# Performance work log

Measured on AMD Instinct MI355X. Metric: run time of the kernel, lower is better.

## Reference

```python
import jax, jax.numpy as jnp
import numpy as np

HEAD_SIZE = 128
N_Q_HEADS = 32
N_KV_HEADS = 8
ROPE_THETA = 1000000.0
RMS_EPS = 1e-6


def rms_norm(x, w, eps=RMS_EPS):
    # normalize over last dim in fp32, like Qwen3RMSNorm
    xf = x.astype(jnp.float32)
    var = jnp.mean(xf * xf, axis=-1, keepdims=True)
    return w * (xf * jax.lax.rsqrt(var + eps)).astype(x.dtype)


def rope_cache(T, dim, theta=ROPE_THETA):
    half = dim // 2
    inv_freq = 1.0 / theta ** (jnp.arange(half, dtype=jnp.float32) / half)
    freqs = jnp.arange(T, dtype=jnp.float32)[:, None] * inv_freq[None, :]  # [T, half]
    emb = jnp.concatenate([freqs, freqs], axis=-1)  # [T, dim]
    return jnp.cos(emb), jnp.sin(emb)


def rotate_half(x):
    x1, x2 = jnp.split(x, 2, axis=-1)
    return jnp.concatenate([-x2, x1], axis=-1)


def setup_inputs() -> dict:
    key = jax.random.key(0)
    ks = jax.random.split(key, 5)
    B, T, C = 2, 2048, 4096
    s = 0.02
    return {
        "hidden_states": jax.random.normal(ks[0], (B, T, C), jnp.float32),
        "wq": jax.random.normal(ks[1], (N_Q_HEADS * HEAD_SIZE, C), jnp.float32) * s,
        "wk": jax.random.normal(ks[2], (N_KV_HEADS * HEAD_SIZE, C), jnp.float32) * s,
        "wv": jax.random.normal(ks[3], (N_KV_HEADS * HEAD_SIZE, C), jnp.float32) * s,
        "wo": jax.random.normal(ks[4], (C, N_Q_HEADS * HEAD_SIZE), jnp.float32) * s,
        "q_norm_w": jnp.ones((HEAD_SIZE,), jnp.float32),
        "k_norm_w": jnp.ones((HEAD_SIZE,), jnp.float32),
    }


def reference(hidden_states, wq, wk, wv, wo, q_norm_w, k_norm_w):
    B, T, C = hidden_states.shape
    D = HEAD_SIZE
    groups = N_Q_HEADS // N_KV_HEADS
    scale = D ** -0.5

    # projections -> [B, H, T, D]
    q = (hidden_states @ wq.T).reshape(B, T, N_Q_HEADS, D)
    k = (hidden_states @ wk.T).reshape(B, T, N_KV_HEADS, D)
    v = (hidden_states @ wv.T).reshape(B, T, N_KV_HEADS, D)

    q = rms_norm(q, q_norm_w).transpose(0, 2, 1, 3)
    k = rms_norm(k, k_norm_w).transpose(0, 2, 1, 3)
    v = v.transpose(0, 2, 1, 3)

    cos, sin = rope_cache(T, D)  # [T, D]
    cos = cos[None, None]  # broadcast over batch, heads
    sin = sin[None, None]
    q = q * cos + rotate_half(q) * sin
    k = k * cos + rotate_half(k) * sin

    # GQA repeat_kv: [B, Hkv, T, D] -> [B, Hq, T, D]
    k = jnp.repeat(k, groups, axis=1)
    v = jnp.repeat(v, groups, axis=1)

    # causal SDPA
    scores = jnp.einsum("bhqd,bhkd->bhqk", q, k) * scale
    causal = jnp.tril(jnp.ones((T, T), bool))
    scores = jnp.where(causal[None, None], scores, -jnp.inf)
    probs = jax.nn.softmax(scores, axis=-1)
    attn = jnp.einsum("bhqk,bhkd->bhqd", probs, v)

    attn = attn.transpose(0, 2, 1, 3).reshape(B, T, N_Q_HEADS * D)
    return attn @ wo.T
```

## Files before the change

kernel.cpp:

```cpp
#include <hip/hip_runtime.h>
#include <math.h>

typedef unsigned short u16;
typedef __attribute__((ext_vector_type(8))) short short8;
typedef __attribute__((ext_vector_type(4))) float f32x4;
typedef __attribute__((ext_vector_type(16))) float f32x16;

#define AS1 __attribute__((address_space(1)))
#define AS3 __attribute__((address_space(3)))

__device__ __forceinline__ void gload_lds16(const u16* g, u16* l) {
  __builtin_amdgcn_global_load_lds((AS1 void*)g, (AS3 void*)l, 16, 0, 0);
}

__device__ __forceinline__ float bf2f(u16 u) {
  union { unsigned i; float f; } c; c.i = ((unsigned)u) << 16; return c.f;
}
__device__ __forceinline__ u16 f2bf(float f) {
  union { float f; unsigned i; } c; c.f = f;
  unsigned r = c.i + 0x7fffu + ((c.i >> 16) & 1u);
  return (u16)(r >> 16);
}

__global__ __launch_bounds__(256)
void cvt_f32_bf16_k(const float* __restrict__ src, u16* __restrict__ dst, int n8)
{
  int i = blockIdx.x * blockDim.x + threadIdx.x;
  const int stride = gridDim.x * blockDim.x;
  for (; i < n8; i += stride) {
    float4 a = ((const float4*)src)[2 * i];
    float4 b = ((const float4*)src)[2 * i + 1];
    short8 o;
    o[0] = (short)f2bf(a.x); o[1] = (short)f2bf(a.y);
    o[2] = (short)f2bf(a.z); o[3] = (short)f2bf(a.w);
    o[4] = (short)f2bf(b.x); o[5] = (short)f2bf(b.y);
    o[6] = (short)f2bf(b.z); o[7] = (short)f2bf(b.w);
    ((short8*)dst)[i] = o;
  }
}

__global__ __launch_bounds__(256)
void cvt_batch4(const float* __restrict__ s0, u16* __restrict__ d0,
                const float* __restrict__ s1, u16* __restrict__ d1,
                const float* __restrict__ s2, u16* __restrict__ d2,
                const float* __restrict__ s3, u16* __restrict__ d3)
{
  int i = blockIdx.x * blockDim.x + threadIdx.x;
  const int stride = gridDim.x * blockDim.x;
  for (; i < 5242880; i += stride) {
    const float* s; u16* d; int j;
    if (i < 2097152)      { s = s0; d = d0; j = i; }
    else if (i < 4194304) { s = s1; d = d1; j = i - 2097152; }
    else if (i < 4718592) { s = s2; d = d2; j = i - 4194304; }
    else                  { s = s3; d = d3; j = i - 4718592; }
    float4 a = ((const float4*)s)[2 * j];
    float4 b = ((const float4*)s)[2 * j + 1];
    short8 o;
    o[0] = (short)f2bf(a.x); o[1] = (short)f2bf(a.y);
    o[2] = (short)f2bf(a.z); o[3] = (short)f2bf(a.w);
    o[4] = (short)f2bf(b.x); o[5] = (short)f2bf(b.y);
    o[6] = (short)f2bf(b.z); o[7] = (short)f2bf(b.w);
    ((short8*)d)[j] = o;
  }
}

#define MFMA16(a, b, c) __builtin_amdgcn_mfma_f32_16x16x32_bf16((a), (b), (c), 0, 0, 0)

#define STAGE_H(panel, h, t, ldsb)                                          \
  { const u16* s_ = (panel) + (size_t)((h) * 128) * 4096 + (t) * 64;        \
    gload_lds16(s_,                   (ldsb) + ldst0);                      \
    gload_lds16(s_ + (size_t)64*4096, (ldsb) + 4096 + ldst0); }

#define PHASE(MB, STAGE_STMT, TAIL)                                         \
  {                                                                         \
    short8 a0k0 = *(const short8*)(aB + (MB)*1024 + aoff0);                 \
    short8 a0k1 = *(const short8*)(aB + (MB)*1024 + (aoff0 ^ 32));          \
    short8 a1k0 = *(const short8*)(aB + ((MB)+1)*1024 + aoff0);             \
    short8 a1k1 = *(const short8*)(aB + ((MB)+1)*1024 + (aoff0 ^ 32));      \
    STAGE_STMT                                                              \
    __builtin_amdgcn_s_barrier();                                           \
    asm volatile("s_waitcnt lgkmcnt(0)" ::: "memory");                      \
    __builtin_amdgcn_s_setprio(1);                                          \
    _Pragma("unroll")                                                       \
    for (int n = 0; n < 4; ++n) {                                           \
      acc[(MB)][n]   = MFMA16(a0k0, br[n][0], acc[(MB)][n]);                \
      acc[(MB)][n]   = MFMA16(a0k1, br[n][1], acc[(MB)][n]);                \
      acc[(MB)+1][n] = MFMA16(a1k0, br[n][0], acc[(MB)+1][n]);              \
      acc[(MB)+1][n] = MFMA16(a1k1, br[n][1], acc[(MB)+1][n]);              \
    }                                                                       \
    __builtin_amdgcn_s_setprio(0);                                          \
    TAIL                                                                    \
    __builtin_amdgcn_s_barrier();                                           \
  }

#define KTILE(BUF, T)                                                       \
  {                                                                         \
    const u16* aB = sA + (BUF) * 16384 + wr * 8192;                         \
    const u16* bB = sB + (BUF) * 16384 + (wc >> 1) * 8192;                  \
    u16* aO = sA + ((BUF) ^ 1) * 16384;                                     \
    u16* bO = sB + (BUF) * 16384;                                           \
    const bool st1 = (T) + 1 < NT, st2 = (T) + 2 < NT;                      \
    short8 br[4][2];                                                        \
    _Pragma("unroll")                                                       \
    for (int n = 0; n < 4; ++n) {                                           \
      br[n][0] = *(const short8*)(bB + n * 1024 + boff0);                   \
      br[n][1] = *(const short8*)(bB + n * 1024 + (boff0 ^ 32));            \
    }                                                                       \
    PHASE(0, if (st1) STAGE_H(aS, 0, (T) + 1, aO);, ;)                      \
    PHASE(2, if (st1) STAGE_H(aS, 1, (T) + 1, aO + 8192);, ;)               \
    PHASE(4, if (st2) STAGE_H(bS, 0, (T) + 2, bO);, ;)                      \
    PHASE(6, if (st2) STAGE_H(bS, 1, (T) + 2, bO + 8192);,                  \
          if ((T) < NT - 2) { asm volatile("s_waitcnt vmcnt(4)" ::: "memory"); } \
          else              { asm volatile("s_waitcnt vmcnt(0)" ::: "memory"); }) \
  }

template<int MODE, typename OutT>
__global__ __launch_bounds__(512, 2)
void gemm256(const u16* __restrict__ A, const u16* __restrict__ W0,
             const u16* __restrict__ W1, const u16* __restrict__ W2,
             OutT* __restrict__ C)
{
  constexpr int K = 4096;
  constexpr int NT = K / 64;
  constexpr int LDC = (MODE == 0) ? 6144 : 4096;
  constexpr int NBM = 16;
  constexpr int NBN = (MODE == 0) ? 24 : 16;
  constexpr int NWG = NBM * NBN;

  __shared__ __align__(16) u16 sA[2 * 16384];
  __shared__ __align__(16) u16 sB[2 * 16384];

  const int tid = threadIdx.x;
  const int wid = tid >> 6, lane = tid & 63;
  const int g = lane >> 4, li = lane & 15;
  const int wr = wid >> 2, wc = wid & 3;

  const int bid = blockIdx.x;
  const int wg = (bid & 7) * (NWG / 8) + (bid >> 3);
  const int bm = wg % NBM, bn = wg / NBM;
  const int n0 = bn * 256;

  const u16* Wp; int nrow0;
  if (MODE == 0) {
    if (n0 < 4096)      { Wp = W0; nrow0 = n0; }
    else if (n0 < 5120) { Wp = W1; nrow0 = n0 - 4096; }
    else                { Wp = W2; nrow0 = n0 - 5120; }
  } else { Wp = W0; nrow0 = n0; }

  const int r0 = tid >> 3;
  const int sc0 = (tid & 7) ^ (r0 & 7);
  const u16* aS = A  + (size_t)(bm * 256 + r0) * K + sc0 * 8;
  const u16* bS = Wp + (size_t)(nrow0   + r0) * K + sc0 * 8;
  const int ldst0 = wid * 512;

  const int aoff0 = li * 64 + ((g ^ (li & 7)) * 8);
  const int boff0 = (wc & 1) * 4096 + aoff0;

  f32x4 acc[8][4] = {};

  STAGE_H(bS, 0, 0, sB);
  STAGE_H(bS, 1, 0, sB + 8192);
  STAGE_H(aS, 0, 0, sA);
  STAGE_H(aS, 1, 0, sA + 8192);
  STAGE_H(bS, 0, 1, sB + 16384);
  STAGE_H(bS, 1, 1, sB + 24576);
  asm volatile("s_waitcnt vmcnt(4)" ::: "memory");
  __builtin_amdgcn_s_barrier();

  for (int t = 0; t < NT; t += 2) {
    KTILE(0, t)
    KTILE(1, t + 1)
  }

#pragma unroll
  for (int m = 0; m < 8; ++m)
#pragma unroll
    for (int n = 0; n < 4; ++n)
#pragma unroll
      for (int j = 0; j < 4; ++j) {
        int row = bm * 256 + wr * 128 + m * 16 + g * 4 + j;
        int col = n0 + wc * 64 + n * 16 + li;
        float v = acc[m][n][j];
        if constexpr (sizeof(OutT) == 2) C[(size_t)row * LDC + col] = (OutT)f2bf(v);
        else                             C[(size_t)row * LDC + col] = (OutT)v;
      }
}

__global__ __launch_bounds__(256)
void norm_rope(const u16* __restrict__ qkv, const float* __restrict__ qw,
               const float* __restrict__ kw, u16* __restrict__ Qo,
               u16* __restrict__ Ko)
{
  const int tid = threadIdx.x;
  const int wid = tid >> 6, l = tid & 63;
  const int idx = blockIdx.x * 4 + wid;

  const u16* src; const float* w; u16* dst; int t;
  if (idx < 131072) {
    int row = idx >> 5, h = idx & 31;
    int b = row >> 11; t = row & 2047;
    src = qkv + (size_t)row * 6144 + h * 128;
    w = qw;
    dst = Qo + (((size_t)(b * 32 + h)) * 2048 + t) * 128;
  } else {
    int j = idx - 131072;
    int row = j >> 3, hk = j & 7;
    int b = row >> 11; t = row & 2047;
    src = qkv + (size_t)row * 6144 + 4096 + hk * 128;
    w = kw;
    dst = Ko + (((size_t)(b * 8 + hk)) * 2048 + t) * 128;
  }

  float x1 = bf2f(src[l]), x2 = bf2f(src[l + 64]);
  float ss = x1 * x1 + x2 * x2;
#pragma unroll
  for (int off = 32; off; off >>= 1) ss += __shfl_xor(ss, off);
  float rn = rsqrtf(ss * (1.0f / 128.0f) + 1e-6f);
  float y1 = x1 * rn * w[l];
  float y2 = x2 * rn * w[l + 64];

  float ang = (float)t * expf((float)l * -0.21586735246819178f);
  float c = cosf(ang), s = sinf(ang);
  dst[l]      = f2bf(y1 * c - y2 * s);
  dst[l + 64] = f2bf(y2 * c + y1 * s);
}

__global__ __launch_bounds__(256)
void transpose_v(const u16* __restrict__ qkv, u16* __restrict__ Vt)
{
  const int tblk = blockIdx.x, bh = blockIdx.y;
  const int b = bh >> 3, hk = bh & 7;
  const int tid = threadIdx.x;
  __shared__ __align__(16) u16 tile[64][136];

#pragma unroll
  for (int r = 0; r < 4; ++r) {
    int u = tid + r * 256;
    int row = u >> 4, cu = u & 15;
    short8 v = *(const short8*)(qkv + (size_t)(b * 2048 + tblk * 64 + row) * 6144
                                + 5120 + hk * 128 + cu * 8);
    *(short8*)(&tile[row][cu * 8]) = v;
  }
  __syncthreads();
#pragma unroll
  for (int it = 0; it < 4; ++it) {
    int u = tid + it * 256;
    int d = u & 127, tg = u >> 7;
    short8 wv8;
#pragma unroll
    for (int j = 0; j < 8; ++j) wv8[j] = (short)tile[tg * 8 + j][d];
    *(short8*)(Vt + ((size_t)(b * 8 + hk) * 128 + d) * 2048 + tblk * 64 + tg * 8) = wv8;
  }
}

__global__ __launch_bounds__(256, 2)
void attn_fwd(const u16* __restrict__ Q, const u16* __restrict__ Kc,
              const u16* __restrict__ Vt, u16* __restrict__ O)
{
  const int qt = 15 - (int)blockIdx.x;
  const int bh = blockIdx.y;
  const int b = bh >> 5, h = bh & 31, hkv = h >> 2;
  const int tid = threadIdx.x, wid = tid >> 6;
  const int lane = tid & 63, ql = lane & 31, hi = lane >> 5;

  __shared__ __align__(16) u16 sK[2][64 * 128];
  __shared__ __align__(16) u16 sV[2][128 * 64];

  const u16* Kb = Kc + ((size_t)(b * 8 + hkv)) * 2048 * 128;
  const u16* Vb = Vt + ((size_t)(b * 8 + hkv)) * 128 * 2048;

  const int kr0 = tid >> 4;
  const u16* kSrc = Kb + (size_t)kr0 * 128 + (((tid & 15) ^ (kr0 & 7)) * 8);
  const int vr0 = tid >> 3;
  const u16* vSrc = Vb + (size_t)vr0 * 2048 + (((tid & 7) ^ (vr0 & 7)) * 8);
  u16* const kDst = (u16*)sK[0] + wid * 512;
  u16* const vDst = (u16*)sV[0] + wid * 512;

  const int qg = qt * 128 + wid * 32 + ql;
  const u16* qrow = Q + ((size_t)(b * 32 + h) * 2048 + qg) * 128;
  short8 qf[8];
#pragma unroll
  for (int m = 0; m < 8; ++m) qf[m] = *(const short8*)(qrow + m * 16 + hi * 8);

  f32x16 oacc[4] = {};
  float mrun = -INFINITY, lrun = 0.f;
  const float scale = 0.08838834764831845f;
  const int nt = 2 * qt + 2;

#pragma unroll
  for (int p = 0; p < 4; ++p) {
    gload_lds16(kSrc + p * 2048,  kDst + p * 2048);
    gload_lds16(vSrc + p * 65536, vDst + p * 2048);
  }
  asm volatile("s_waitcnt vmcnt(0)" ::: "memory");
  __builtin_amdgcn_s_barrier();

  int cur = 0;
  for (int kt = 0; kt < nt; ++kt) {
    const int kv0 = kt * 64;
    if (kt + 1 < nt) {
      const u16* ks = kSrc + (size_t)(kv0 + 64) * 128;
      const u16* vs = vSrc + (kv0 + 64);
      u16* kd = kDst + (cur ^ 1) * 8192;
      u16* vd = vDst + (cur ^ 1) * 8192;
#pragma unroll
      for (int p = 0; p < 4; ++p) {
        gload_lds16(ks + p * 2048,  kd + p * 2048);
        gload_lds16(vs + p * 65536, vd + p * 2048);
      }
    }
    const u16* sKc = sK[cur];
    const u16* sVc = sV[cur];

    f32x16 P0 = {}, P1 = {};
    __builtin_amdgcn_s_setprio(1);
#pragma unroll
    for (int m = 0; m < 8; ++m) {
      const int c0 = ((m * 2 + hi) ^ (ql & 7)) * 8;
      short8 k0 = *(const short8*)(sKc + ql * 128 + c0);
      short8 k1 = *(const short8*)(sKc + (32 + ql) * 128 + c0);
      P0 = __builtin_amdgcn_mfma_f32_32x32x16_bf16(k0, qf[m], P0, 0, 0, 0);
      P1 = __builtin_amdgcn_mfma_f32_32x32x16_bf16(k1, qf[m], P1, 0, 0, 0);
    }
    __builtin_amdgcn_s_setprio(0);

#pragma unroll
    for (int r = 0; r < 16; ++r) {
      const int kvl = (r & 3) + 8 * (r >> 2) + 4 * hi;
      float v0 = P0[r] * scale; if (kv0 + kvl > qg)      v0 = -INFINITY; P0[r] = v0;
      float v1 = P1[r] * scale; if (kv0 + 32 + kvl > qg) v1 = -INFINITY; P1[r] = v1;
    }

    float pmax = -INFINITY;
#pragma unroll
    for (int r = 0; r < 16; ++r) pmax = fmaxf(pmax, fmaxf(P0[r], P1[r]));
    pmax = fmaxf(pmax, __shfl_xor(pmax, 32));

    if (!__all(pmax - mrun <= 8.f)) {
      float mnew = fmaxf(mrun, pmax);
      float corr = __expf(mrun - mnew);
      lrun *= corr;
      mrun = mnew;
#pragma unroll
      for (int r = 0; r < 16; ++r) {
        int qidx = (r & 3) + 8 * (r >> 2) + 4 * hi;
        float cr = __shfl(corr, qidx);
#pragma unroll
        for (int dt = 0; dt < 4; ++dt) oacc[dt][r] *= cr;
      }
    }

    float psum = 0.f;
#pragma unroll
    for (int r = 0; r < 16; ++r) {
      float e0 = __expf(P0[r] - mrun); P0[r] = e0; psum += e0;
      float e1 = __expf(P1[r] - mrun); P1[r] = e1; psum += e1;
    }
    psum += __shfl_xor(psum, 32);
    lrun += psum;

    __builtin_amdgcn_s_setprio(1);
#pragma unroll
    for (int s = 0; s < 4; ++s) {
      const int R0 = 8 * (s & 1), R1 = R0 + 4;
      float a0 = (s < 2) ? P0[R0 + 0] : P1[R0 + 0];
      float a1 = (s < 2) ? P0[R0 + 1] : P1[R0 + 1];
      float a2 = (s < 2) ? P0[R0 + 2] : P1[R0 + 2];
      float a3 = (s < 2) ? P0[R0 + 3] : P1[R0 + 3];
      float b0 = (s < 2) ? P0[R1 + 0] : P1[R1 + 0];
      float b1 = (s < 2) ? P0[R1 + 1] : P1[R1 + 1];
      float b2 = (s < 2) ? P0[R1 + 2] : P1[R1 + 2];
      float b3 = (s < 2) ? P0[R1 + 3] : P1[R1 + 3];
      unsigned y0, y1, z0, z1;
      asm("v_cvt_pk_bf16_f32 %0, %1, %2" : "=v"(y0) : "v"(a0), "v"(a1));
      asm("v_cvt_pk_bf16_f32 %0, %1, %2" : "=v"(z0) : "v"(b0), "v"(b1));
      asm("v_cvt_pk_bf16_f32 %0, %1, %2" : "=v"(y1) : "v"(a2), "v"(a3));
      asm("v_cvt_pk_bf16_f32 %0, %1, %2" : "=v"(z1) : "v"(b2), "v"(b3));
      asm("v_permlane32_swap_b32 %0, %1" : "+v"(y0), "+v"(z0));
      asm("v_permlane32_swap_b32 %0, %1" : "+v"(y1), "+v"(z1));
      union { unsigned u[4]; short8 v; } pa;
      pa.u[0] = y0; pa.u[1] = y1; pa.u[2] = z0; pa.u[3] = z1;
#pragma unroll
      for (int dt = 0; dt < 4; ++dt) {
        const int c = ((s * 2 + hi) ^ (ql & 7)) * 8;
        short8 vf = *(const short8*)(sVc + (dt * 32 + ql) * 64 + c);
        oacc[dt] = __builtin_amdgcn_mfma_f32_32x32x16_bf16(pa.v, vf, oacc[dt], 0, 0, 0);
      }
    }
    __builtin_amdgcn_s_setprio(0);

    asm volatile("s_waitcnt lgkmcnt(0)" ::: "memory");
    asm volatile("s_waitcnt vmcnt(0)" ::: "memory");
    __builtin_amdgcn_s_barrier();
    cur ^= 1;
  }

  float inv = 1.f / lrun;
  const int qbase = b * 2048 + qt * 128 + wid * 32;
#pragma unroll
  for (int r = 0; r < 16; ++r) {
    const int qidx = (r & 3) + 8 * (r >> 2) + 4 * hi;
    float ir = __shfl(inv, qidx);
    size_t base = (size_t)(qbase + qidx) * 4096 + h * 128 + ql;
#pragma unroll
    for (int dt = 0; dt < 4; ++dt)
      O[base + dt * 32] = f2bf(oacc[dt][r] * ir);
  }
}

extern "C" void kernel_launch(void* const* d_in, const int* in_sizes, int n_in,
                              void* d_out, int out_size, void* d_ws, size_t ws_size,
                              hipStream_t stream) {
  const float* hs  = (const float*)d_in[0];
  const float* wq  = (const float*)d_in[1];
  const float* wk  = (const float*)d_in[2];
  const float* wv  = (const float*)d_in[3];
  const float* wo  = (const float*)d_in[4];
  const float* qnw = (const float*)d_in[5];
  const float* knw = (const float*)d_in[6];
  float* out = (float*)d_out;

  char* ws = (char*)d_ws;
  u16* qkv = (u16*)(ws);
  u16* qr  = (u16*)(ws + 50331648);
  u16* kr  = (u16*)(ws + 83886080);
  u16* vt  = (u16*)(ws + 92274688);
  u16* hsb = (u16*)(ws + 100663296);
  u16* wqb = (u16*)(ws + 134217728);
  u16* wkb = (u16*)(ws + 167772160);
  u16* wvb = (u16*)(ws + 176160768);
  u16* ao  = (u16*)(ws);
  u16* wob = hsb;

  cvt_batch4<<<dim3(2048), dim3(256), 0, stream>>>(hs, hsb, wq, wqb, wk, wkb, wv, wvb);

  gemm256<0, u16><<<dim3(384), dim3(512), 0, stream>>>(hsb, wqb, wkb, wvb, qkv);
  cvt_f32_bf16_k<<<dim3(2048), dim3(256), 0, stream>>>(wo, wob, 16777216 / 8);
  norm_rope<<<dim3(40960), dim3(256), 0, stream>>>(qkv, qnw, knw, qr, kr);
  transpose_v<<<dim3(32, 16), dim3(256), 0, stream>>>(qkv, vt);
  attn_fwd<<<dim3(16, 64), dim3(256), 0, stream>>>(qr, kr, vt, ao);

  gemm256<1, float><<<dim3(256), dim3(512), 0, stream>>>(ao, wob, nullptr, nullptr, out);
}
```

Before: 605.2 us.

## Fuse V transpose into QKV GEMM epilogue and reorder MFMA issue

The QKV GEMM epilogue now writes the V columns directly in transposed [b, hk, d, t] layout as packed 4-element bf16 stores, so the separate transpose_v kernel is removed. This saves one launch and a full read and write of V through global memory. The inner MFMA loop is also reordered so consecutive MFMAs target different accumulators, which shortens back-to-back dependency stalls. The wo conversion launch moves after attention. The transposed stores are strided by 2048 elements, so the V-tile epilogue writes are less coalesced.

```diff
diff --git a/kernel.cpp b/kernel.cpp
--- a/kernel.cpp
+++ b/kernel.cpp
@@ -2,6 +2,7 @@
 #include <math.h>
 
 typedef unsigned short u16;
+typedef __attribute__((ext_vector_type(4))) unsigned short u16x4;
 typedef __attribute__((ext_vector_type(8))) short short8;
 typedef __attribute__((ext_vector_type(4))) float f32x4;
 typedef __attribute__((ext_vector_type(16))) float f32x16;
@@ -82,12 +83,17 @@
     asm volatile("s_waitcnt lgkmcnt(0)" ::: "memory");                      \
     __builtin_amdgcn_s_setprio(1);                                          \
     _Pragma("unroll")                                                       \
-    for (int n = 0; n < 4; ++n) {                                           \
+    for (int n = 0; n < 4; ++n)                                             \
       acc[(MB)][n]   = MFMA16(a0k0, br[n][0], acc[(MB)][n]);                \
+    _Pragma("unroll")                                                       \
+    for (int n = 0; n < 4; ++n)                                             \
+      acc[(MB)+1][n] = MFMA16(a1k0, br[n][0], acc[(MB)+1][n]);              \
+    _Pragma("unroll")                                                       \
+    for (int n = 0; n < 4; ++n)                                             \
       acc[(MB)][n]   = MFMA16(a0k1, br[n][1], acc[(MB)][n]);                \
-      acc[(MB)+1][n] = MFMA16(a1k0, br[n][0], acc[(MB)+1][n]);              \
+    _Pragma("unroll")                                                       \
+    for (int n = 0; n < 4; ++n)                                             \
       acc[(MB)+1][n] = MFMA16(a1k1, br[n][1], acc[(MB)+1][n]);              \
-    }                                                                       \
     __builtin_amdgcn_s_setprio(0);                                          \
     TAIL                                                                    \
     __builtin_amdgcn_s_barrier();                                           \
@@ -118,7 +124,7 @@
 __global__ __launch_bounds__(512, 2)
 void gemm256(const u16* __restrict__ A, const u16* __restrict__ W0,
              const u16* __restrict__ W1, const u16* __restrict__ W2,
-             OutT* __restrict__ C)
+             OutT* __restrict__ C, u16* __restrict__ VT)
 {
   constexpr int K = 4096;
   constexpr int NT = K / 64;
@@ -172,18 +178,34 @@
     KTILE(1, t + 1)
   }
 
-#pragma unroll
-  for (int m = 0; m < 8; ++m)
-#pragma unroll
-    for (int n = 0; n < 4; ++n)
-#pragma unroll
-      for (int j = 0; j < 4; ++j) {
-        int row = bm * 256 + wr * 128 + m * 16 + g * 4 + j;
-        int col = n0 + wc * 64 + n * 16 + li;
-        float v = acc[m][n][j];
-        if constexpr (sizeof(OutT) == 2) C[(size_t)row * LDC + col] = (OutT)f2bf(v);
-        else                             C[(size_t)row * LDC + col] = (OutT)v;
+  if (MODE == 0 && n0 >= 5120) {
+#pragma unroll
+    for (int m = 0; m < 8; ++m)
+#pragma unroll
+      for (int n = 0; n < 4; ++n) {
+        int row0 = bm * 256 + wr * 128 + m * 16 + g * 4;
+        int dcol = (n0 - 5120) + wc * 64 + n * 16 + li;
+        int bb = row0 >> 11, t0 = row0 & 2047;
+        int hk = dcol >> 7, dd = dcol & 127;
+        u16x4 pk;
+#pragma unroll
+        for (int j = 0; j < 4; ++j) pk[j] = f2bf(acc[m][n][j]);
+        *(u16x4*)(VT + ((size_t)((bb * 8 + hk) * 128 + dd)) * 2048 + t0) = pk;
       }
+  } else {
+#pragma unroll
+    for (int m = 0; m < 8; ++m)
+#pragma unroll
+      for (int n = 0; n < 4; ++n)
+#pragma unroll
+        for (int j = 0; j < 4; ++j) {
+          int row = bm * 256 + wr * 128 + m * 16 + g * 4 + j;
+          int col = n0 + wc * 64 + n * 16 + li;
+          float v = acc[m][n][j];
+          if constexpr (sizeof(OutT) == 2) C[(size_t)row * LDC + col] = (OutT)f2bf(v);
+          else                             C[(size_t)row * LDC + col] = (OutT)v;
+        }
+  }
 }
 
 __global__ __launch_bounds__(256)
@@ -223,34 +245,6 @@
   float c = cosf(ang), s = sinf(ang);
   dst[l]      = f2bf(y1 * c - y2 * s);
   dst[l + 64] = f2bf(y2 * c + y1 * s);
-}
-
-__global__ __launch_bounds__(256)
-void transpose_v(const u16* __restrict__ qkv, u16* __restrict__ Vt)
-{
-  const int tblk = blockIdx.x, bh = blockIdx.y;
-  const int b = bh >> 3, hk = bh & 7;
-  const int tid = threadIdx.x;
-  __shared__ __align__(16) u16 tile[64][136];
-
-#pragma unroll
-  for (int r = 0; r < 4; ++r) {
-    int u = tid + r * 256;
-    int row = u >> 4, cu = u & 15;
-    short8 v = *(const short8*)(qkv + (size_t)(b * 2048 + tblk * 64 + row) * 6144
-                                + 5120 + hk * 128 + cu * 8);
-    *(short8*)(&tile[row][cu * 8]) = v;
-  }
-  __syncthreads();
-#pragma unroll
-  for (int it = 0; it < 4; ++it) {
-    int u = tid + it * 256;
-    int d = u & 127, tg = u >> 7;
-    short8 wv8;
-#pragma unroll
-    for (int j = 0; j < 8; ++j) wv8[j] = (short)tile[tg * 8 + j][d];
-    *(short8*)(Vt + ((size_t)(b * 8 + hk) * 128 + d) * 2048 + tblk * 64 + tg * 8) = wv8;
-  }
 }
 
 __global__ __launch_bounds__(256, 2)
@@ -434,11 +428,10 @@
 
   cvt_batch4<<<dim3(2048), dim3(256), 0, stream>>>(hs, hsb, wq, wqb, wk, wkb, wv, wvb);
 
-  gemm256<0, u16><<<dim3(384), dim3(512), 0, stream>>>(hsb, wqb, wkb, wvb, qkv);
+  gemm256<0, u16><<<dim3(384), dim3(512), 0, stream>>>(hsb, wqb, wkb, wvb, qkv, vt);
+  norm_rope<<<dim3(40960), dim3(256), 0, stream>>>(qkv, qnw, knw, qr, kr);
+  attn_fwd<<<dim3(16, 64), dim3(256), 0, stream>>>(qr, kr, vt, ao);
+
   cvt_f32_bf16_k<<<dim3(2048), dim3(256), 0, stream>>>(wo, wob, 16777216 / 8);
-  norm_rope<<<dim3(40960), dim3(256), 0, stream>>>(qkv, qnw, knw, qr, kr);
-  transpose_v<<<dim3(32, 16), dim3(256), 0, stream>>>(qkv, vt);
-  attn_fwd<<<dim3(16, 64), dim3(256), 0, stream>>>(qr, kr, vt, ao);
-
-  gemm256<1, float><<<dim3(256), dim3(512), 0, stream>>>(ao, wob, nullptr, nullptr, out);
-}
+  gemm256<1, float><<<dim3(256), dim3(512), 0, stream>>>(ao, wob, nullptr, nullptr, out, nullptr);
+}
```

Result: no change. 605.6 us (+0.1%).
